# Optimization experiments

Measured on AMD Instinct MI355X. Metric: run time of the kernel, lower is better.

Reference implementation:

```python
import jax, jax.numpy as jnp
import numpy as np

DIM = 1024
HEADS = 16
DIM_HEAD = 64
INNER = HEADS * DIM_HEAD  # 1024
B, N = 4, 1024
SCALE = DIM_HEAD ** -0.5


def _layernorm(t, g, b, eps=1e-5):
    mu = jnp.mean(t, axis=-1, keepdims=True)
    var = jnp.var(t, axis=-1, keepdims=True)
    return (t - mu) * jax.lax.rsqrt(var + eps) * g + b


def setup_inputs() -> dict:
    key = jax.random.key(0)
    ks = jax.random.split(key, 8)
    return {
        "x": jax.random.normal(ks[0], (B, N, DIM), dtype=jnp.float32),
        "y": jax.random.normal(ks[1], (B, N, DIM), dtype=jnp.float32),
        "gx": jnp.ones((DIM,), jnp.float32),
        "bx": jnp.zeros((DIM,), jnp.float32),
        "gy": jnp.ones((DIM,), jnp.float32),
        "by": jnp.zeros((DIM,), jnp.float32),
        "Wqkv_x": jax.random.normal(ks[2], (DIM, 3 * INNER), jnp.float32) * 0.02,
        "Wqkv_y": jax.random.normal(ks[3], (DIM, 3 * INNER), jnp.float32) * 0.02,
        "Wout_x": jax.random.normal(ks[4], (INNER, DIM), jnp.float32) * 0.02,
        "bout_x": jnp.zeros((DIM,), jnp.float32),
        "Wout_y": jax.random.normal(ks[5], (INNER, DIM), jnp.float32) * 0.02,
        "bout_y": jnp.zeros((DIM,), jnp.float32),
    }


def _split_heads(t):
    b, n, _ = t.shape
    return t.reshape(b, n, HEADS, DIM_HEAD).transpose(0, 2, 1, 3)  # b h n d


def reference(x, y, gx, bx, gy, by, Wqkv_x, Wqkv_y, Wout_x, bout_x, Wout_y, bout_y):
    xn = _layernorm(x, gx, bx)
    yn = _layernorm(y, gy, by)
    qx, kx, vx = [_split_heads(t) for t in jnp.split(xn @ Wqkv_x, 3, axis=-1)]
    qy, ky, vy = [_split_heads(t) for t in jnp.split(yn @ Wqkv_y, 3, axis=-1)]
    # concat along HEADS dim -> 2h heads; each stream's heads attend within that stream
    q = jnp.concatenate([qx, qy], axis=1)
    k = jnp.concatenate([kx, ky], axis=1)
    v = jnp.concatenate([vx, vy], axis=1)
    dots = jnp.einsum('bhid,bhjd->bhij', q, k) * SCALE  # [B, 2h, N, N]
    attn = jax.nn.softmax(dots, axis=-1)
    out = jnp.einsum('bhij,bhjd->bhid', attn, v)  # [B, 2h, N, d]
    xo = out[:, :HEADS]  # original code uses the x-chunk for BOTH outputs (faithful)
    xo = xo.transpose(0, 2, 1, 3).reshape(xo.shape[0], xo.shape[2], INNER)  # b n (h d)
    out_x = xo @ Wout_x + bout_x
    out_y = xo @ Wout_y + bout_y
    return (out_x, out_y)
```

## Files before the change

kernel.cpp:

```cpp
#include <hip/hip_runtime.h>

typedef __attribute__((ext_vector_type(8))) short s16x8;
typedef __attribute__((ext_vector_type(4))) float f32x4;
typedef unsigned short u16;

#define DEV __device__ __forceinline__

DEV u16 f2bf(float f) {
    unsigned u = __builtin_bit_cast(unsigned, f);
    unsigned r = u + 0x7fffu + ((u >> 16) & 1u);
    return (u16)(r >> 16);
}

DEV float exp2a(float x) {
    float r;
    asm("v_exp_f32 %0, %1" : "=v"(r) : "v"(x));
    return r;
}

DEV unsigned cvtpk(float lo, float hi) {
    unsigned r;
    asm("v_cvt_pk_bf16_f32 %0, %1, %2" : "=v"(r) : "v"(lo), "v"(hi));
    return r;
}

DEV void gload_lds16(const void* g, void* l) {
    __builtin_amdgcn_global_load_lds(
        (const __attribute__((address_space(1))) unsigned int*)g,
        (__attribute__((address_space(3))) unsigned int*)l, 16, 0, 0);
}

DEV f32x4 mfma16(s16x8 a, s16x8 b, f32x4 c) {
    return __builtin_amdgcn_mfma_f32_16x16x32_bf16(a, b, c, 0, 0, 0);
}

template <int N>
DEV void vmwait() {
    asm volatile("s_waitcnt vmcnt(%0)" ::"n"(N) : "memory");
}

__global__ __launch_bounds__(256) void ln_kernel(const float* __restrict__ x,
                                                 const float* __restrict__ g,
                                                 const float* __restrict__ b,
                                                 u16* __restrict__ xn) {
    const int row = blockIdx.x, t = threadIdx.x;
    const float4 v = *(const float4*)(x + (size_t)row * 1024 + t * 4);
    float s1 = v.x + v.y + v.z + v.w;
    float s2 = v.x * v.x + v.y * v.y + v.z * v.z + v.w * v.w;
#pragma unroll
    for (int d = 1; d < 64; d <<= 1) {
        s1 += __shfl_xor(s1, d);
        s2 += __shfl_xor(s2, d);
    }
    __shared__ float red[8];
    if ((t & 63) == 0) { red[(t >> 6) * 2] = s1; red[(t >> 6) * 2 + 1] = s2; }
    __syncthreads();
    s1 = red[0] + red[2] + red[4] + red[6];
    s2 = red[1] + red[3] + red[5] + red[7];
    const float mu = s1 * (1.0f / 1024.0f);
    const float var = s2 * (1.0f / 1024.0f) - mu * mu;
    const float rs = rsqrtf(var + 1e-5f);
    const float4 gv = *(const float4*)(g + t * 4);
    const float4 bv = *(const float4*)(b + t * 4);
    ushort4 o;
    o.x = f2bf((v.x - mu) * rs * gv.x + bv.x);
    o.y = f2bf((v.y - mu) * rs * gv.y + bv.y);
    o.z = f2bf((v.z - mu) * rs * gv.z + bv.z);
    o.w = f2bf((v.w - mu) * rs * gv.w + bv.w);
    *(ushort4*)(xn + (size_t)row * 1024 + t * 4) = o;
}

__global__ __launch_bounds__(256) void transpose_w(const float* __restrict__ src,
                                                   u16* __restrict__ dst, int ld) {
    __shared__ float tile[64][68];
    const int t = threadIdx.x;
    const int n0 = blockIdx.x * 64, k0 = blockIdx.y * 64;
    const int kl = t >> 4, nl = (t & 15) * 4;
#pragma unroll
    for (int p = 0; p < 4; ++p) {
        float4 v = *(const float4*)(src + (size_t)(k0 + kl + p * 16) * ld + n0 + nl);
        tile[kl + p * 16][nl + 0] = v.x;
        tile[kl + p * 16][nl + 1] = v.y;
        tile[kl + p * 16][nl + 2] = v.z;
        tile[kl + p * 16][nl + 3] = v.w;
    }
    __syncthreads();
    const int nl2 = t >> 2, kc = (t & 3) * 16;
    __align__(16) u16 tmp[16];
#pragma unroll
    for (int j = 0; j < 16; ++j) tmp[j] = f2bf(tile[kc + j][nl2]);
    u16* d = dst + (size_t)(n0 + nl2) * 1024 + k0 + kc;
    ((uint4*)d)[0] = ((const uint4*)tmp)[0];
    ((uint4*)d)[1] = ((const uint4*)tmp)[1];
}

__global__ __launch_bounds__(256) void transpose_v(const u16* __restrict__ V,
                                                   u16* __restrict__ Vt) {
    __shared__ u16 tile[64][72];
    const int t = threadIdx.x;
    const int j0 = blockIdx.x * 64;
    const int bh = blockIdx.y;
    const u16* src = V + (size_t)bh * 65536;
    const int jl = t >> 4, dl = (t & 15) * 4;
#pragma unroll
    for (int p = 0; p < 4; ++p) {
        ushort4 v = *(const ushort4*)(src + (size_t)(j0 + jl + p * 16) * 64 + dl);
        *(ushort4*)&tile[jl + p * 16][dl] = v;
    }
    __syncthreads();
    const int dl2 = t >> 2, jc = (t & 3) * 16;
    __align__(16) u16 tmp[16];
#pragma unroll
    for (int j = 0; j < 16; ++j) tmp[j] = tile[jc + j][dl2];
    u16* d = Vt + (size_t)bh * 65536 + (size_t)dl2 * 1024 + j0 + jc;
    ((uint4*)d)[0] = ((const uint4*)tmp)[0];
    ((uint4*)d)[1] = ((const uint4*)tmp)[1];
}

template <int BN, int WM, int EPI>
__global__ __launch_bounds__(512, 2) void gemm8(const u16* __restrict__ A,
                                                const u16* __restrict__ B,
                                                u16* __restrict__ Qb, u16* __restrict__ Kb,
                                                u16* __restrict__ Vb,
                                                const float* __restrict__ bx,
                                                const float* __restrict__ by,
                                                float* __restrict__ out, int NBX) {
    constexpr int BM = 256, WN = 8 / WM;
    constexpr int TM = BM / WM, TN = BN / WN;
    constexpr int MQ = TM / 32, NQ = TN / 32;
    constexpr int HA = TM / 2, HB = TN / 2;
    constexpr int CHA = 1024;
    constexpr int CHB = BN * 4;
    constexpr int GA = 2, GB = CHB / 512;
    constexpr int NI = 8;

    __shared__ __align__(16) u16 As[2 * 2 * CHA * 8];
    __shared__ __align__(16) u16 Bs[2 * 2 * CHB * 8];

    const int tid = threadIdx.x, lane = tid & 63;
    const int wave = tid >> 6;
    const int wm = wave / WN, wn = wave % WN;
    const int lr = lane & 15, cg = lane >> 4;

    const int nwg = NBX * 16;
    const int bid = blockIdx.x;
    const int bid2 = (bid & 7) * (nwg >> 3) + (bid >> 3);
    const int bxi = bid2 % NBX, byi = bid2 / NBX;
    const int m0 = byi * 256, n0 = bxi * BN;

    const u16* __restrict__ Ag = A + (size_t)m0 * 1024;
    const u16* __restrict__ Bg = B + (size_t)n0 * 1024;

    f32x4 acc[2 * MQ][2 * NQ] = {};

#define STG_A(b, h, t)                                                              \
    do {                                                                            \
        _Pragma("unroll") for (int u = 0; u < GA; ++u) {                            \
            const int idx = u * 512 + tid;                                          \
            const int loc = idx >> 3, pp = idx & 7;                                 \
            const int row = (loc & (HA - 1)) | ((h)*HA) | ((loc / HA) * 2 * HA);    \
            gload_lds16(Ag + (size_t)row * 1024 + (t)*64 + ((pp ^ (row & 7)) << 3), \
                        &As[(((b)*2 + (h)) * CHA + idx) * 8]);                      \
        }                                                                           \
    } while (0)
#define STG_B(b, h, t)                                                              \
    do {                                                                            \
        _Pragma("unroll") for (int u = 0; u < GB; ++u) {                            \
            const int idx = u * 512 + tid;                                          \
            const int loc = idx >> 3, pp = idx & 7;                                 \
            const int row = (loc & (HB - 1)) | ((h)*HB) | ((loc / HB) * 2 * HB);    \
            gload_lds16(Bg + (size_t)row * 1024 + (t)*64 + ((pp ^ (row & 7)) << 3), \
                        &Bs[(((b)*2 + (h)) * CHB + idx) * 8]);                      \
        }                                                                           \
    } while (0)

#define LDA(bb, lm, dst)                                                            \
    _Pragma("unroll") for (int mf = 0; mf < MQ; ++mf)                               \
        _Pragma("unroll") for (int ks = 0; ks < 2; ++ks)                            \
            dst[mf][ks] = *(const s16x8*)&As[((((bb)*2 + (lm)) * CHA) +             \
                                              (mf * 16 + lr + wm * HA) * 8 +        \
                                              ((cg + ks * 4) ^ (lr & 7))) * 8];

#define LDB(bb, ln, dst)                                                            \
    _Pragma("unroll") for (int nf = 0; nf < NQ; ++nf)                               \
        _Pragma("unroll") for (int ks = 0; ks < 2; ++ks)                            \
            dst[nf][ks] = *(const s16x8*)&Bs[((((bb)*2 + (ln)) * CHB) +             \
                                              (nf * 16 + lr + wn * HB) * 8 +        \
                                              ((cg + ks * 4) ^ (lr & 7))) * 8];

#define MM(lm, ln, A_, B_)                                                          \
    __builtin_amdgcn_s_setprio(1);                                                  \
    _Pragma("unroll") for (int mf = 0; mf < MQ; ++mf)                               \
        _Pragma("unroll") for (int nf = 0; nf < NQ; ++nf)                           \
            _Pragma("unroll") for (int ks = 0; ks < 2; ++ks)                        \
                acc[(lm)*MQ + mf][(ln)*NQ + nf] = mfma16(                           \
                    A_[mf][ks], B_[nf][ks], acc[(lm)*MQ + mf][(ln)*NQ + nf]);       \
    __builtin_amdgcn_s_setprio(0);

#define BAR() asm volatile("s_barrier" ::: "memory")

    STG_A(0, 0, 0);
    STG_A(0, 1, 0);
    STG_B(0, 0, 0);
    STG_B(0, 1, 0);
    STG_A(1, 0, 1);
    STG_B(1, 0, 1);
    vmwait<GA + GB>();
    BAR();

    s16x8 va[MQ][2];
    s16x8 vb[2][NQ][2];

#pragma unroll 1
    for (int i = 0; i < NI - 1; ++i) {
        const int t1 = 2 * i + 1, t2 = 2 * i + 2, t3 = 2 * i + 3;
        LDA(0, 0, va); LDB(0, 0, vb[0]); STG_A(1, 1, t1); BAR(); MM(0, 0, va, vb[0]);
        LDB(0, 1, vb[1]);                STG_B(1, 1, t1); BAR(); MM(0, 1, va, vb[1]);
        LDA(0, 1, va);                   STG_A(0, 0, t2); BAR(); MM(1, 0, va, vb[0]);
        STG_B(0, 0, t2); vmwait<GA + GB>();               BAR(); MM(1, 1, va, vb[1]);
        LDA(1, 0, va); LDB(1, 0, vb[0]); STG_A(0, 1, t2); BAR(); MM(0, 0, va, vb[0]);
        LDB(1, 1, vb[1]);                STG_B(0, 1, t2); BAR(); MM(0, 1, va, vb[1]);
        LDA(1, 1, va);                   STG_A(1, 0, t3); BAR(); MM(1, 0, va, vb[0]);
        STG_B(1, 0, t3); vmwait<GA + GB>();               BAR(); MM(1, 1, va, vb[1]);
    }
    LDA(0, 0, va); LDB(0, 0, vb[0]); STG_A(1, 1, 15); BAR(); MM(0, 0, va, vb[0]);
    LDB(0, 1, vb[1]);                STG_B(1, 1, 15); BAR(); MM(0, 1, va, vb[1]);
    LDA(0, 1, va);                                    BAR(); MM(1, 0, va, vb[0]);
    vmwait<0>();                                      BAR(); MM(1, 1, va, vb[1]);
    LDA(1, 0, va); LDB(1, 0, vb[0]); MM(0, 0, va, vb[0]);
    LDB(1, 1, vb[1]);                MM(0, 1, va, vb[1]);
    LDA(1, 1, va);                   MM(1, 0, va, vb[0]);
    MM(1, 1, va, vb[1]);

#undef STG_A
#undef STG_B
#undef LDA
#undef LDB
#undef MM
#undef BAR

#pragma unroll
    for (int am = 0; am < 2 * MQ; ++am) {
        const int lm = am / MQ, mf = am % MQ;
        const int rowb = m0 + wm * TM + lm * HA + mf * 16 + cg * 4;
#pragma unroll
        for (int an = 0; an < 2 * NQ; ++an) {
            const int ln = an / NQ, nf = an % NQ;
            const int col = n0 + wn * TN + ln * HB + nf * 16 + lr;
            if (EPI == 0) {
                const int which = col >> 10, hd = col & 1023;
                const int h = hd >> 6, dd = hd & 63;
                u16* dst = (which == 0) ? Qb : (which == 1) ? Kb : Vb;
                const float sc = (which == 0) ? 0.18033688011112042f : 1.0f;
#pragma unroll
                for (int r = 0; r < 4; ++r) {
                    const int tk = rowb + r;
                    const int bb2 = tk >> 10, ii = tk & 1023;
                    dst[(size_t)(((bb2 << 4) + h) * 1024 + ii) * 64 + dd] =
                        f2bf(acc[am][an][r] * sc);
                }
            } else {
                float bias;
                float* ob;
                if (col < 1024) { bias = bx[col]; ob = out + col; }
                else { bias = by[col - 1024]; ob = out + 4194304 + (col - 1024); }
#pragma unroll
                for (int r = 0; r < 4; ++r)
                    ob[(size_t)(rowb + r) * 1024] = acc[am][an][r] + bias;
            }
        }
    }
}

__global__ __launch_bounds__(256) void attn_kernel(const u16* __restrict__ Q,
                                                   const u16* __restrict__ Kg,
                                                   const u16* __restrict__ Vt,
                                                   u16* __restrict__ xo) {
    __shared__ __align__(16) u16 Ks[2][64 * 64];
    __shared__ __align__(16) u16 Vs[2][64 * 64];
    __shared__ __align__(16) u16 Ps[4][32 * 64];
    const int tid = threadIdx.x, lane = tid & 63, w = tid >> 6;
    const int bh = blockIdx.x >> 3, qblk = blockIdx.x & 7;
    const u16* Qh = Q + (size_t)bh * 65536;
    const u16* Kh = Kg + (size_t)bh * 65536;
    const u16* Vh = Vt + (size_t)bh * 65536;
    const int lr = lane & 15, cg = lane >> 4;
    const int q0 = qblk * 128 + w * 32;
    u16* Pw = &Ps[w][0];

    s16x8 qf[2][2];
#pragma unroll
    for (int qg = 0; qg < 2; ++qg)
#pragma unroll
        for (int ks = 0; ks < 2; ++ks)
            qf[qg][ks] =
                *(const s16x8*)(Qh + (size_t)(q0 + qg * 16 + lr) * 64 + ks * 32 + cg * 8);

    f32x4 o[2][4] = {};
    float l_s[2] = {0.f, 0.f};
    float m_s[2] = {-3e38f, -3e38f};
    int ba[4];
#pragma unroll
    for (int r = 0; r < 4; ++r) ba[r] = (cg * 4 + r) * 4;

#define STAGEKV(bufi, kv0)                                                               \
    do {                                                                                 \
        _Pragma("unroll") for (int i = 0; i < 2; ++i) {                                  \
            int idx = i * 256 + tid;                                                     \
            int row = idx >> 3, p = idx & 7;                                             \
            gload_lds16(Kh + (size_t)((kv0) + row) * 64 + ((p ^ (row & 7)) << 3),        \
                        &Ks[bufi][idx * 8]);                                             \
            gload_lds16(Vh + (size_t)row * 1024 + (kv0) + ((p ^ (row & 7)) << 3),        \
                        &Vs[bufi][idx * 8]);                                             \
        }                                                                                \
    } while (0)

    STAGEKV(0, 0);
    asm volatile("s_waitcnt vmcnt(0)" ::: "memory");
    __syncthreads();

    for (int t = 0; t < 16; ++t) {
        const int buf = t & 1;
        if (t < 15) STAGEKV(buf ^ 1, (t + 1) * 64);

        f32x4 s[2][4] = {};
#pragma unroll
        for (int fn = 0; fn < 4; ++fn) {
            const int r = fn * 16 + lr;
#pragma unroll
            for (int ks = 0; ks < 2; ++ks) {
                const int c = cg + ks * 4;
                s16x8 kf = *(const s16x8*)&Ks[buf][r * 64 + ((c ^ (r & 7)) << 3)];
                s[0][fn] = mfma16(kf, qf[0][ks], s[0][fn]);
                s[1][fn] = mfma16(kf, qf[1][ks], s[1][fn]);
            }
        }

#pragma unroll
        for (int qg = 0; qg < 2; ++qg) {
            float tm = -3e38f;
#pragma unroll
            for (int fn = 0; fn < 4; ++fn)
#pragma unroll
                for (int r = 0; r < 4; ++r) tm = fmaxf(tm, s[qg][fn][r]);
            tm = fmaxf(tm, __shfl_xor(tm, 16));
            tm = fmaxf(tm, __shfl_xor(tm, 32));
            if (!__all(tm <= m_s[qg] + 8.0f)) {
                const float mn = fmaxf(m_s[qg], tm);
                const float corr = exp2a(m_s[qg] - mn);
                m_s[qg] = mn;
                l_s[qg] *= corr;
                f32x4 corr_o;
#pragma unroll
                for (int r = 0; r < 4; ++r)
                    corr_o[r] = __builtin_bit_cast(
                        float,
                        __builtin_amdgcn_ds_bpermute(ba[r], __builtin_bit_cast(int, corr)));
#pragma unroll
                for (int fd = 0; fd < 4; ++fd) o[qg][fd] *= corr_o;
            }
            const float mn = m_s[qg];
            float rs = 0.f;
            const int prow = (qg * 16 + lr) * 64;
#pragma unroll
            for (int fn = 0; fn < 4; ++fn) {
                const float p0 = exp2a(s[qg][fn][0] - mn);
                const float p1 = exp2a(s[qg][fn][1] - mn);
                const float p2 = exp2a(s[qg][fn][2] - mn);
                const float p3 = exp2a(s[qg][fn][3] - mn);
                rs += (p0 + p1) + (p2 + p3);
                uint2 dd;
                dd.x = cvtpk(p0, p1);
                dd.y = cvtpk(p2, p3);
                *(uint2*)(Pw + prow + (((2 * fn + (cg >> 1)) ^ (lr & 7)) << 3) +
                          ((cg & 1) << 2)) = dd;
            }
            rs += __shfl_xor(rs, 16);
            rs += __shfl_xor(rs, 32);
            l_s[qg] += rs;
        }

        s16x8 pf[2][2];
#pragma unroll
        for (int qg = 0; qg < 2; ++qg)
#pragma unroll
            for (int ks = 0; ks < 2; ++ks)
                pf[qg][ks] = *(const s16x8*)(Pw + (qg * 16 + lr) * 64 +
                                             (((4 * ks + cg) ^ (lr & 7)) << 3));
#pragma unroll
        for (int fd = 0; fd < 4; ++fd) {
            const int rr = fd * 16 + lr;
#pragma unroll
            for (int ks = 0; ks < 2; ++ks) {
                const int c = cg + ks * 4;
                s16x8 vf = *(const s16x8*)&Vs[buf][rr * 64 + ((c ^ (rr & 7)) << 3)];
                o[0][fd] = mfma16(pf[0][ks], vf, o[0][fd]);
                o[1][fd] = mfma16(pf[1][ks], vf, o[1][fd]);
            }
        }
        asm volatile("s_waitcnt vmcnt(0)" ::: "memory");
        __syncthreads();
    }
#undef STAGEKV

    const int b = bh >> 4, h = bh & 15;
#pragma unroll
    for (int qg = 0; qg < 2; ++qg) {
        f32x4 inv;
#pragma unroll
        for (int r = 0; r < 4; ++r) {
            const float lq = __builtin_bit_cast(
                float, __builtin_amdgcn_ds_bpermute(ba[r], __builtin_bit_cast(int, l_s[qg])));
            inv[r] = 1.0f / lq;
        }
#pragma unroll
        for (int r = 0; r < 4; ++r) {
            const int qrow = q0 + qg * 16 + cg * 4 + r;
#pragma unroll
            for (int fd = 0; fd < 4; ++fd)
                xo[(size_t)(b * 1024 + qrow) * 1024 + h * 64 + fd * 16 + lr] =
                    f2bf(o[qg][fd][r] * inv[r]);
        }
    }
}

extern "C" void kernel_launch(void* const* d_in, const int* in_sizes, int n_in,
                              void* d_out, int out_size, void* d_ws, size_t ws_size,
                              hipStream_t stream) {
    const float* x = (const float*)d_in[0];
    const float* gx = (const float*)d_in[2];
    const float* bxv = (const float*)d_in[3];
    const float* Wqkv = (const float*)d_in[6];
    const float* Woutx = (const float*)d_in[8];
    const float* boutx = (const float*)d_in[9];
    const float* Wouty = (const float*)d_in[10];
    const float* bouty = (const float*)d_in[11];
    float* out = (float*)d_out;

    u16* ws = (u16*)d_ws;
    u16* xn = ws;
    u16* wqkv_t = xn + 4096 * 1024;
    u16* wout_t = wqkv_t + 3072 * 1024;
    u16* Qb = wout_t + 2048 * 1024;
    u16* Kb = Qb + 64 * 1024 * 64;
    u16* Vb = Kb + 64 * 1024 * 64;
    u16* Vtb = Vb + 64 * 1024 * 64;
    u16* xob = Vtb + 64 * 1024 * 64;

    ln_kernel<<<4096, 256, 0, stream>>>(x, gx, bxv, xn);
    transpose_w<<<dim3(48, 16), 256, 0, stream>>>(Wqkv, wqkv_t, 3072);
    transpose_w<<<dim3(16, 16), 256, 0, stream>>>(Woutx, wout_t, 1024);
    transpose_w<<<dim3(16, 16), 256, 0, stream>>>(Wouty, wout_t + 1024 * 1024, 1024);
    gemm8<256, 2, 0><<<192, 512, 0, stream>>>(xn, wqkv_t, Qb, Kb, Vb, nullptr, nullptr,
                                              nullptr, 12);
    transpose_v<<<dim3(16, 64), 256, 0, stream>>>(Vb, Vtb);
    attn_kernel<<<512, 256, 0, stream>>>(Qb, Kb, Vtb, xob);
    gemm8<128, 4, 1><<<256, 512, 0, stream>>>(xob, wout_t, nullptr, nullptr, nullptr,
                                              boutx, bouty, out, 16);
}
```

Measured before the change: 119.3 us.

## Double KV tile to 128 in attention and add phase barriers in GEMM

The attention kernel now stages 128 keys/values per iteration instead of 64, halving the loop trip count and the number of sync/wait points, and processes P@V in two 64-wide halves that reuse the per-wave P buffer. The GEMM main loop gets an extra barrier plus an lgkmcnt wait and sched_barrier around each MFMA phase, so LDS reads finish before the matrix math and the compiler cannot interleave them. The larger tiles double LDS use for K/V, which may reduce occupancy and raise register pressure. The extra barriers in the GEMM may add stall overhead.

```diff
diff --git a/kernel.cpp b/kernel.cpp
--- a/kernel.cpp
+++ b/kernel.cpp
@@ -198,6 +198,11 @@
     __builtin_amdgcn_s_setprio(0);
 
 #define BAR() asm volatile("s_barrier" ::: "memory")
+#define PH_PRE()                                                                    \
+    BAR();                                                                          \
+    asm volatile("s_waitcnt lgkmcnt(0)" ::: "memory");                              \
+    __builtin_amdgcn_sched_barrier(0)
+#define PH_POST() BAR()
 
     STG_A(0, 0, 0);
     STG_A(0, 1, 0);
@@ -209,28 +214,40 @@
     BAR();
 
     s16x8 va[MQ][2];
-    s16x8 vb[2][NQ][2];
+    s16x8 vb0[NQ][2], vb1[NQ][2];
 
 #pragma unroll 1
     for (int i = 0; i < NI - 1; ++i) {
         const int t1 = 2 * i + 1, t2 = 2 * i + 2, t3 = 2 * i + 3;
-        LDA(0, 0, va); LDB(0, 0, vb[0]); STG_A(1, 1, t1); BAR(); MM(0, 0, va, vb[0]);
-        LDB(0, 1, vb[1]);                STG_B(1, 1, t1); BAR(); MM(0, 1, va, vb[1]);
-        LDA(0, 1, va);                   STG_A(0, 0, t2); BAR(); MM(1, 0, va, vb[0]);
-        STG_B(0, 0, t2); vmwait<GA + GB>();               BAR(); MM(1, 1, va, vb[1]);
-        LDA(1, 0, va); LDB(1, 0, vb[0]); STG_A(0, 1, t2); BAR(); MM(0, 0, va, vb[0]);
-        LDB(1, 1, vb[1]);                STG_B(0, 1, t2); BAR(); MM(0, 1, va, vb[1]);
-        LDA(1, 1, va);                   STG_A(1, 0, t3); BAR(); MM(1, 0, va, vb[0]);
-        STG_B(1, 0, t3); vmwait<GA + GB>();               BAR(); MM(1, 1, va, vb[1]);
-    }
-    LDA(0, 0, va); LDB(0, 0, vb[0]); STG_A(1, 1, 15); BAR(); MM(0, 0, va, vb[0]);
-    LDB(0, 1, vb[1]);                STG_B(1, 1, 15); BAR(); MM(0, 1, va, vb[1]);
-    LDA(0, 1, va);                                    BAR(); MM(1, 0, va, vb[0]);
-    vmwait<0>();                                      BAR(); MM(1, 1, va, vb[1]);
-    LDA(1, 0, va); LDB(1, 0, vb[0]); MM(0, 0, va, vb[0]);
-    LDB(1, 1, vb[1]);                MM(0, 1, va, vb[1]);
-    LDA(1, 1, va);                   MM(1, 0, va, vb[0]);
-    MM(1, 1, va, vb[1]);
+        LDA(0, 0, va); LDB(0, 0, vb0); STG_A(1, 1, t1);
+        PH_PRE(); MM(0, 0, va, vb0); PH_POST();
+        LDB(0, 1, vb1); STG_B(1, 1, t1);
+        PH_PRE(); MM(0, 1, va, vb1); PH_POST();
+        LDA(0, 1, va); STG_A(0, 0, t2);
+        PH_PRE(); MM(1, 0, va, vb0); PH_POST();
+        STG_B(0, 0, t2); vmwait<GA + GB>();
+        PH_PRE(); MM(1, 1, va, vb1); PH_POST();
+        LDA(1, 0, va); LDB(1, 0, vb0); STG_A(0, 1, t2);
+        PH_PRE(); MM(0, 0, va, vb0); PH_POST();
+        LDB(1, 1, vb1); STG_B(0, 1, t2);
+        PH_PRE(); MM(0, 1, va, vb1); PH_POST();
+        LDA(1, 1, va); STG_A(1, 0, t3);
+        PH_PRE(); MM(1, 0, va, vb0); PH_POST();
+        STG_B(1, 0, t3); vmwait<GA + GB>();
+        PH_PRE(); MM(1, 1, va, vb1); PH_POST();
+    }
+    LDA(0, 0, va); LDB(0, 0, vb0); STG_A(1, 1, 15);
+    PH_PRE(); MM(0, 0, va, vb0); PH_POST();
+    LDB(0, 1, vb1); STG_B(1, 1, 15);
+    PH_PRE(); MM(0, 1, va, vb1); PH_POST();
+    LDA(0, 1, va);
+    PH_PRE(); MM(1, 0, va, vb0); PH_POST();
+    vmwait<0>();
+    PH_PRE(); MM(1, 1, va, vb1); PH_POST();
+    LDA(1, 0, va); LDB(1, 0, vb0); MM(0, 0, va, vb0);
+    LDB(1, 1, vb1); MM(0, 1, va, vb1);
+    LDA(1, 1, va); MM(1, 0, va, vb0);
+    MM(1, 1, va, vb1);
 
 #undef STG_A
 #undef STG_B
@@ -238,6 +255,8 @@
 #undef LDB
 #undef MM
 #undef BAR
+#undef PH_PRE
+#undef PH_POST
 
 #pragma unroll
     for (int am = 0; am < 2 * MQ; ++am) {
@@ -276,8 +295,8 @@
                                                    const u16* __restrict__ Kg,
                                                    const u16* __restrict__ Vt,
                                                    u16* __restrict__ xo) {
-    __shared__ __align__(16) u16 Ks[2][64 * 64];
-    __shared__ __align__(16) u16 Vs[2][64 * 64];
+    __shared__ __align__(16) u16 Ks[2][128 * 64];
+    __shared__ __align__(16) u16 Vs[2][64 * 128];
     __shared__ __align__(16) u16 Ps[4][32 * 64];
     const int tid = threadIdx.x, lane = tid & 63, w = tid >> 6;
     const int bh = blockIdx.x >> 3, qblk = blockIdx.x & 7;
@@ -305,13 +324,17 @@
 
 #define STAGEKV(bufi, kv0)                                                               \
     do {                                                                                 \
-        _Pragma("unroll") for (int i = 0; i < 2; ++i) {                                  \
+        _Pragma("unroll") for (int i = 0; i < 4; ++i) {                                  \
             int idx = i * 256 + tid;                                                     \
             int row = idx >> 3, p = idx & 7;                                             \
             gload_lds16(Kh + (size_t)((kv0) + row) * 64 + ((p ^ (row & 7)) << 3),        \
                         &Ks[bufi][idx * 8]);                                             \
-            gload_lds16(Vh + (size_t)row * 1024 + (kv0) + ((p ^ (row & 7)) << 3),        \
-                        &Vs[bufi][idx * 8]);                                             \
+        }                                                                                \
+        _Pragma("unroll") for (int i = 0; i < 4; ++i) {                                  \
+            int idx = i * 256 + tid;                                                     \
+            int row = idx >> 4, p = idx & 15;                                            \
+            int srcc = ((p & 8) | ((p & 7) ^ (row & 7))) << 3;                           \
+            gload_lds16(Vh + (size_t)row * 1024 + (kv0) + srcc, &Vs[bufi][idx * 8]);     \
         }                                                                                \
     } while (0)
 
@@ -319,13 +342,13 @@
     asm volatile("s_waitcnt vmcnt(0)" ::: "memory");
     __syncthreads();
 
-    for (int t = 0; t < 16; ++t) {
+    for (int t = 0; t < 8; ++t) {
         const int buf = t & 1;
-        if (t < 15) STAGEKV(buf ^ 1, (t + 1) * 64);
-
-        f32x4 s[2][4] = {};
-#pragma unroll
-        for (int fn = 0; fn < 4; ++fn) {
+        if (t < 7) STAGEKV(buf ^ 1, (t + 1) * 128);
+
+        f32x4 s[2][8] = {};
+#pragma unroll
+        for (int fn = 0; fn < 8; ++fn) {
             const int r = fn * 16 + lr;
 #pragma unroll
             for (int ks = 0; ks < 2; ++ks) {
@@ -336,11 +359,12 @@
             }
         }
 
+        float rs_[2] = {0.f, 0.f};
 #pragma unroll
         for (int qg = 0; qg < 2; ++qg) {
             float tm = -3e38f;
 #pragma unroll
-            for (int fn = 0; fn < 4; ++fn)
+            for (int fn = 0; fn < 8; ++fn)
 #pragma unroll
                 for (int r = 0; r < 4; ++r) tm = fmaxf(tm, s[qg][fn][r]);
             tm = fmaxf(tm, __shfl_xor(tm, 16));
@@ -359,44 +383,54 @@
 #pragma unroll
                 for (int fd = 0; fd < 4; ++fd) o[qg][fd] *= corr_o;
             }
-            const float mn = m_s[qg];
-            float rs = 0.f;
-            const int prow = (qg * 16 + lr) * 64;
-#pragma unroll
-            for (int fn = 0; fn < 4; ++fn) {
-                const float p0 = exp2a(s[qg][fn][0] - mn);
-                const float p1 = exp2a(s[qg][fn][1] - mn);
-                const float p2 = exp2a(s[qg][fn][2] - mn);
-                const float p3 = exp2a(s[qg][fn][3] - mn);
-                rs += (p0 + p1) + (p2 + p3);
-                uint2 dd;
-                dd.x = cvtpk(p0, p1);
-                dd.y = cvtpk(p2, p3);
-                *(uint2*)(Pw + prow + (((2 * fn + (cg >> 1)) ^ (lr & 7)) << 3) +
-                          ((cg & 1) << 2)) = dd;
+        }
+
+#pragma unroll
+        for (int h = 0; h < 2; ++h) {
+#pragma unroll
+            for (int qg = 0; qg < 2; ++qg) {
+                const float mn = m_s[qg];
+                const int prow = (qg * 16 + lr) * 64;
+#pragma unroll
+                for (int f = 0; f < 4; ++f) {
+                    const float p0 = exp2a(s[qg][h * 4 + f][0] - mn);
+                    const float p1 = exp2a(s[qg][h * 4 + f][1] - mn);
+                    const float p2 = exp2a(s[qg][h * 4 + f][2] - mn);
+                    const float p3 = exp2a(s[qg][h * 4 + f][3] - mn);
+                    rs_[qg] += (p0 + p1) + (p2 + p3);
+                    uint2 dd;
+                    dd.x = cvtpk(p0, p1);
+                    dd.y = cvtpk(p2, p3);
+                    *(uint2*)(Pw + prow + (((2 * f + (cg >> 1)) ^ (lr & 7)) << 3) +
+                              ((cg & 1) << 2)) = dd;
+                }
             }
+            s16x8 pf[2][2];
+#pragma unroll
+            for (int qg = 0; qg < 2; ++qg)
+#pragma unroll
+                for (int ks = 0; ks < 2; ++ks)
+                    pf[qg][ks] = *(const s16x8*)(Pw + (qg * 16 + lr) * 64 +
+                                                 (((4 * ks + cg) ^ (lr & 7)) << 3));
+#pragma unroll
+            for (int fd = 0; fd < 4; ++fd) {
+                const int rr = fd * 16 + lr;
+#pragma unroll
+                for (int ks = 0; ks < 2; ++ks) {
+                    const int c = cg + ks * 4;
+                    s16x8 vf = *(const s16x8*)&Vs[buf][rr * 128 + h * 64 +
+                                                       ((c ^ (rr & 7)) << 3)];
+                    o[0][fd] = mfma16(pf[0][ks], vf, o[0][fd]);
+                    o[1][fd] = mfma16(pf[1][ks], vf, o[1][fd]);
+                }
+            }
+        }
+#pragma unroll
+        for (int qg = 0; qg < 2; ++qg) {
+            float rs = rs_[qg];
             rs += __shfl_xor(rs, 16);
             rs += __shfl_xor(rs, 32);
             l_s[qg] += rs;
-        }
-
-        s16x8 pf[2][2];
-#pragma unroll
-        for (int qg = 0; qg < 2; ++qg)
-#pragma unroll
-            for (int ks = 0; ks < 2; ++ks)
-                pf[qg][ks] = *(const s16x8*)(Pw + (qg * 16 + lr) * 64 +
-                                             (((4 * ks + cg) ^ (lr & 7)) << 3));
-#pragma unroll
-        for (int fd = 0; fd < 4; ++fd) {
-            const int rr = fd * 16 + lr;
-#pragma unroll
-            for (int ks = 0; ks < 2; ++ks) {
-                const int c = cg + ks * 4;
-                s16x8 vf = *(const s16x8*)&Vs[buf][rr * 64 + ((c ^ (rr & 7)) << 3)];
-                o[0][fd] = mfma16(pf[0][ks], vf, o[0][fd]);
-                o[1][fd] = mfma16(pf[1][ks], vf, o[1][fd]);
-            }
         }
         asm volatile("s_waitcnt vmcnt(0)" ::: "memory");
         __syncthreads();
```

Result: slower. 132.9 us (+11.4%).
